# Performance work log

Hardware: AMD Instinct MI355X
Metric: run time of the kernel (lower is better)

## Reference

```python
import jax, jax.numpy as jnp
import numpy as np

N, D, K = 500000, 64, 256
INIT_COUNT = 100  # torch module initializes counts to 100 per cluster


def setup_inputs() -> dict:
    key = jax.random.key(0)
    k1, k2 = jax.random.split(key)
    embedded = jax.random.normal(k1, (N, D), dtype=jnp.float32)
    centers = jax.random.normal(k2, (K, D), dtype=jnp.float32)
    counts = jnp.ones((K,), dtype=jnp.int32) * INIT_COUNT
    return {"embedded": embedded, "centers": centers, "counts": counts}


def reference(embedded, centers, counts):
    # predict_hard: squared euclidean cdist + argmin over clusters
    x2 = jnp.sum(embedded * embedded, axis=1, keepdims=True)          # [N,1]
    c2 = jnp.sum(centers * centers, axis=1)                           # [K]
    dist = x2 - 2.0 * jnp.einsum('nd,kd->nk', embedded, centers) + c2  # [N,K]
    labels = jnp.argmin(dist, axis=1).astype(jnp.int32)               # [N]

    # dcn_loss: gather assigned center, squared diff, sum / N
    diff = embedded - centers[labels]                                 # [N,D]
    loss = jnp.sum(diff * diff) / embedded.shape[0]

    # update_centroids: the sequential running-mean update
    #   center = (1 - 1/count) * center + (1/count) * x  (count incremented per sample)
    # telescopes exactly to a segment-sum form:
    #   new_center_c = (counts_old[c]*center_c + sum_{i: label_i=c} x_i) / (counts_old[c] + n_c)
    n_clusters = centers.shape[0]
    seg_sum = jax.ops.segment_sum(embedded, labels, num_segments=n_clusters)  # [K,D]
    seg_cnt = jax.ops.segment_sum(jnp.ones_like(labels), labels, num_segments=n_clusters)  # [K] int32
    new_counts = counts + seg_cnt
    old_w = counts.astype(embedded.dtype)[:, None]
    new_w = new_counts.astype(embedded.dtype)[:, None]
    new_centers = (old_w * centers + seg_sum) / new_w
    return labels, loss, new_centers, new_counts
```

## Files before the change

kernel.cpp:

```cpp
#include <hip/hip_runtime.h>


typedef __attribute__((ext_vector_type(8))) short bf16x8;
typedef __attribute__((ext_vector_type(4))) float f32x4;

constexpr int K = 256;
constexpr int D = 64;
constexpr int BLK = 768;
constexpr int GRID = 256;
constexpr int WPB = BLK / 64;

struct alignas(16) PackW { unsigned int w[4]; };

#define DS_ADD_F32(addr32, val) \
  asm volatile("ds_add_f32 %0, %1" :: "v"(addr32), "v"(val))

__device__ __forceinline__ unsigned int pack_hi(unsigned int a, unsigned int b) {
  return (a >> 16) | (b & 0xffff0000u);
}

__device__ __forceinline__ void split8(const float4 a, const float4 b,
                                       bf16x8& s0, bf16x8& s1) {
  PackW p0, p1;
  const float fa[8] = {a.x, a.y, a.z, a.w, b.x, b.y, b.z, b.w};
#pragma unroll
  for (int i = 0; i < 4; ++i) {
    float f0 = fa[2 * i], f1 = fa[2 * i + 1];
    unsigned u0 = __float_as_uint(f0), u1 = __float_as_uint(f1);
    p0.w[i] = pack_hi(u0, u1);
    float r0 = f0 - __uint_as_float(u0 & 0xffff0000u);
    float r1 = f1 - __uint_as_float(u1 & 0xffff0000u);
    p1.w[i] = pack_hi(__float_as_uint(r0), __float_as_uint(r1));
  }
  s0 = __builtin_bit_cast(bf16x8, p0);
  s1 = __builtin_bit_cast(bf16x8, p1);
}

__global__ __launch_bounds__(BLK, 3) void assign_kernel(
    const float* __restrict__ emb,
    const float* __restrict__ centers,
    float* __restrict__ out_labels,
    float* __restrict__ ws_seg,
    int*   __restrict__ ws_cnt,
    float* __restrict__ ws_loss,
    int N)
{
  __shared__ __align__(16) unsigned short Bls[2 * K * D];
  __shared__ float seg_lds[K * D];
  __shared__ float hneg_lds[K];
  __shared__ int   cnt_lds[K];
  __shared__ float red[WPB];

  const int tid = threadIdx.x;

  for (int e = tid; e < K * D; e += BLK) {
    int j = e >> 6, d = e & 63;
    float cv = centers[e];
    unsigned u = __float_as_uint(cv);
    unsigned short h0 = (unsigned short)(u >> 16);
    float r = cv - __uint_as_float(u & 0xffff0000u);
    unsigned short h1 = (unsigned short)(__float_as_uint(r) >> 16);
    int nt = j >> 4, c = j & 15;
    int si = nt * 1024 + c * 64 + (d ^ ((c & 7) << 3));
    Bls[si] = h0;
    Bls[16384 + si] = h1;
  }
  if (tid < K) {
    const float4* cp = (const float4*)(centers + tid * D);
    float s = 0.f;
#pragma unroll
    for (int q = 0; q < 16; ++q) {
      float4 v = cp[q];
      s = fmaf(v.x, v.x, s); s = fmaf(v.y, v.y, s);
      s = fmaf(v.z, v.z, s); s = fmaf(v.w, v.w, s);
    }
    hneg_lds[tid] = -0.5f * s;
  }
  for (int e = tid; e < K * D; e += BLK) seg_lds[e] = 0.f;
  if (tid < K) cnt_lds[tid] = 0;
  __syncthreads();

  const int lane = tid & 63;
  const int wid  = tid >> 6;
  const int g    = lane >> 4;
  const int cc   = lane & 15;
  const int swzm = (cc & 7) << 3;
  const int bRow = cc * 64;
  const int bk0 = (8 * g) ^ swzm;
  const int bk1 = (32 + 8 * g) ^ swzm;

  float hreg[16];
#pragma unroll
  for (int nt = 0; nt < 16; ++nt) hreg[nt] = hneg_lds[nt * 16 + cc];

  const unsigned segbase = (unsigned)(size_t)seg_lds;

  float lossS = 0.f;
  float lossX = 0.f;
  const int TILES = N >> 5;
  const int waveGid = blockIdx.x * WPB + wid;

  for (int tile = waveGid; tile < TILES; tile += GRID * WPB) {
    const int base = tile << 5;

    float4 xa[2][2][2];
    bf16x8 fx[2][2][2];
#pragma unroll
    for (int Mt = 0; Mt < 2; ++Mt) {
#pragma unroll
      for (int ks = 0; ks < 2; ++ks) {
        const float4* rp = (const float4*)(emb + (size_t)(base + Mt * 16 + cc) * D + ks * 32 + g * 8);
        xa[Mt][ks][0] = rp[0];
        xa[Mt][ks][1] = rp[1];
      }
#pragma unroll
      for (int ks = 0; ks < 2; ++ks)
        split8(xa[Mt][ks][0], xa[Mt][ks][1], fx[Mt][ks][0], fx[Mt][ks][1]);
#pragma unroll
      for (int ks = 0; ks < 2; ++ks)
#pragma unroll
        for (int h = 0; h < 2; ++h) {
          float4 v = xa[Mt][ks][h];
          lossX = fmaf(v.x, v.x, lossX); lossX = fmaf(v.y, v.y, lossX);
          lossX = fmaf(v.z, v.z, lossX); lossX = fmaf(v.w, v.w, lossX);
        }
    }

    float bE[2][4];
#pragma unroll
    for (int Mt = 0; Mt < 2; ++Mt)
#pragma unroll
      for (int r = 0; r < 4; ++r) bE[Mt][r] = -3.0e38f;

    f32x4 accP[2];
#pragma unroll
    for (int nt = 0; nt < 16; ++nt) {
      float h = hreg[nt];
      f32x4 ci = {h, h, h, h};
      f32x4 a0, a1;
      {
        bf16x8 b0 = *(const bf16x8*)&Bls[nt * 1024 + bRow + bk0];
        bf16x8 b1 = *(const bf16x8*)&Bls[16384 + nt * 1024 + bRow + bk0];
        a0 = __builtin_amdgcn_mfma_f32_16x16x32_bf16(fx[0][0][0], b0, ci, 0, 0, 0);
        a0 = __builtin_amdgcn_mfma_f32_16x16x32_bf16(fx[0][0][1], b0, a0, 0, 0, 0);
        a0 = __builtin_amdgcn_mfma_f32_16x16x32_bf16(fx[0][0][0], b1, a0, 0, 0, 0);
        a1 = __builtin_amdgcn_mfma_f32_16x16x32_bf16(fx[1][0][0], b0, ci, 0, 0, 0);
        a1 = __builtin_amdgcn_mfma_f32_16x16x32_bf16(fx[1][0][1], b0, a1, 0, 0, 0);
        a1 = __builtin_amdgcn_mfma_f32_16x16x32_bf16(fx[1][0][0], b1, a1, 0, 0, 0);
      }
      {
        bf16x8 b0 = *(const bf16x8*)&Bls[nt * 1024 + bRow + bk1];
        bf16x8 b1 = *(const bf16x8*)&Bls[16384 + nt * 1024 + bRow + bk1];
        a0 = __builtin_amdgcn_mfma_f32_16x16x32_bf16(fx[0][1][0], b0, a0, 0, 0, 0);
        a0 = __builtin_amdgcn_mfma_f32_16x16x32_bf16(fx[0][1][1], b0, a0, 0, 0, 0);
        a0 = __builtin_amdgcn_mfma_f32_16x16x32_bf16(fx[0][1][0], b1, a0, 0, 0, 0);
        a1 = __builtin_amdgcn_mfma_f32_16x16x32_bf16(fx[1][1][0], b0, a1, 0, 0, 0);
        a1 = __builtin_amdgcn_mfma_f32_16x16x32_bf16(fx[1][1][1], b0, a1, 0, 0, 0);
        a1 = __builtin_amdgcn_mfma_f32_16x16x32_bf16(fx[1][1][0], b1, a1, 0, 0, 0);
      }
      if (nt > 0) {
        unsigned ib = (unsigned)cc | (unsigned)((nt - 1) << 4);
#pragma unroll
        for (int Mt = 0; Mt < 2; ++Mt)
#pragma unroll
          for (int r = 0; r < 4; ++r) {
            unsigned u = (__float_as_uint(accP[Mt][r]) & 0xFFFFFF00u) | ib;
            bE[Mt][r] = fmaxf(bE[Mt][r], __uint_as_float(u));
          }
      }
      accP[0] = a0; accP[1] = a1;
    }
    {
      unsigned ib = (unsigned)cc | (15u << 4);
#pragma unroll
      for (int Mt = 0; Mt < 2; ++Mt)
#pragma unroll
        for (int r = 0; r < 4; ++r) {
          unsigned u = (__float_as_uint(accP[Mt][r]) & 0xFFFFFF00u) | ib;
          bE[Mt][r] = fmaxf(bE[Mt][r], __uint_as_float(u));
        }
    }

#pragma unroll
    for (int Mt = 0; Mt < 2; ++Mt)
#pragma unroll
      for (int r = 0; r < 4; ++r)
#pragma unroll
        for (int m = 1; m <= 8; m <<= 1)
          bE[Mt][r] = fmaxf(bE[Mt][r], __shfl_xor(bE[Mt][r], m));

#pragma unroll
    for (int Mt = 0; Mt < 2; ++Mt) {
      float v01 = (cc & 1) ? bE[Mt][1] : bE[Mt][0];
      float v23 = (cc & 1) ? bE[Mt][3] : bE[Mt][2];
      float vv  = (cc & 2) ? v23 : v01;
      if (cc < 4) {
        int vi = (int)(__float_as_uint(vv) & 255u);
        out_labels[base + Mt * 16 + g * 4 + cc] = (float)vi;
        lossS += vv;
        atomicAdd(&cnt_lds[vi], 1);
      }
      int srcl = (cc >> 2) << 4;
      float e0 = __shfl(bE[Mt][0], srcl);
      float e1 = __shfl(bE[Mt][1], srcl);
      float e2 = __shfl(bE[Mt][2], srcl);
      float e3 = __shfl(bE[Mt][3], srcl);
      float t01 = (cc & 1) ? e1 : e0;
      float t23 = (cc & 1) ? e3 : e2;
      float er  = (cc & 2) ? t23 : t01;
      int lbl = (int)(__float_as_uint(er) & 255u);
      unsigned sb = segbase + ((unsigned)lbl << 8);
      int sw = lbl & 31;
#pragma unroll
      for (int ks = 0; ks < 2; ++ks)
#pragma unroll
        for (int hf = 0; hf < 2; ++hf) {
          float4 v = xa[Mt][ks][hf];
          int d0 = ks * 32 + 8 * g + hf * 4;
          DS_ADD_F32(sb + (unsigned)(((d0 + 0) ^ sw) << 2), v.x);
          DS_ADD_F32(sb + (unsigned)(((d0 + 1) ^ sw) << 2), v.y);
          DS_ADD_F32(sb + (unsigned)(((d0 + 2) ^ sw) << 2), v.z);
          DS_ADD_F32(sb + (unsigned)(((d0 + 3) ^ sw) << 2), v.w);
        }
    }
  }

  asm volatile("s_waitcnt lgkmcnt(0)" ::: "memory");

  float acc = fmaf(-2.f, lossS, lossX);
#pragma unroll
  for (int off = 32; off > 0; off >>= 1) acc += __shfl_down(acc, off);
  if (lane == 0) red[wid] = acc;
  __syncthreads();
  if (tid == 0) {
    float t = 0.f;
#pragma unroll
    for (int w = 0; w < WPB; ++w) t += red[w];
    unsafeAtomicAdd(ws_loss, t);
  }
  for (int e = tid; e < K * D; e += BLK) {
    int k = e >> 6, d = e & 63;
    unsafeAtomicAdd(&ws_seg[e], seg_lds[(k << 6) + (d ^ (k & 31))]);
  }
  if (tid < K) atomicAdd(&ws_cnt[tid], cnt_lds[tid]);
}

__global__ void finalize_kernel(
    const float* __restrict__ centers,
    const int* __restrict__ counts,
    const float* __restrict__ ws_seg,
    const int* __restrict__ ws_cnt,
    const float* __restrict__ ws_loss,
    float* __restrict__ out_loss,
    float* __restrict__ out_centers,
    float* __restrict__ out_counts,
    int N)
{
  int idx = blockIdx.x * blockDim.x + threadIdx.x;
  if (idx < K * D) {
    int k = idx >> 6;
    float oldw = (float)counts[k];
    float neww = (float)(counts[k] + ws_cnt[k]);
    out_centers[idx] = fmaf(oldw, centers[idx], ws_seg[idx]) / neww;
  }
  if (idx < K) out_counts[idx] = (float)(counts[idx] + ws_cnt[idx]);
  if (idx == 0) out_loss[0] = ws_loss[0] / (float)N;
}

extern "C" void kernel_launch(void* const* d_in, const int* in_sizes, int n_in,
                              void* d_out, int out_size, void* d_ws, size_t ws_size,
                              hipStream_t stream) {
  const float* emb     = (const float*)d_in[0];
  const float* centers = (const float*)d_in[1];
  const int*   counts  = (const int*)d_in[2];

  const int Kn = in_sizes[2];
  const int Dn = in_sizes[1] / Kn;
  const int N  = in_sizes[0] / Dn;

  float* out         = (float*)d_out;
  float* out_labels  = out;
  float* out_loss    = out + N;
  float* out_centers = out + N + 1;
  float* out_counts  = out + N + 1 + (size_t)Kn * Dn;

  float* ws_seg  = (float*)d_ws;
  int*   ws_cnt  = (int*)(ws_seg + (size_t)Kn * Dn);
  float* ws_loss = (float*)(ws_cnt + Kn);

  hipMemsetAsync(d_ws, 0, (size_t)(Kn * Dn + Kn + 1) * sizeof(float), stream);

  hipLaunchKernelGGL(assign_kernel, dim3(GRID), dim3(BLK), 0, stream,
                     emb, centers, out_labels, ws_seg, ws_cnt, ws_loss, N);

  hipLaunchKernelGGL(finalize_kernel, dim3((Kn * Dn + 255) / 256), dim3(256), 0, stream,
                     centers, counts, ws_seg, ws_cnt, ws_loss,
                     out_loss, out_centers, out_counts, N);
}
```

Baseline: 394.5 us.

## Split segment-sum out of assign kernel into separate pass for occupancy

Moves the per-cluster segment sum and count accumulation out of the distance/argmin kernel into a new segsum_kernel that re-reads embeddings and the just-written labels. Removing the 64KB seg_lds buffer from the assign kernel frees LDS, so the kernel can use 1024-thread blocks and a larger grid. The MFMA loop is also simplified by dropping the one-step delayed argmax pipelining. The cost is a second full pass over the 128MB embedding array plus an extra kernel launch.

```diff
diff --git a/kernel.cpp b/kernel.cpp
--- a/kernel.cpp
+++ b/kernel.cpp
@@ -6,9 +6,13 @@
 
 constexpr int K = 256;
 constexpr int D = 64;
-constexpr int BLK = 768;
-constexpr int GRID = 256;
-constexpr int WPB = BLK / 64;
+
+constexpr int BLK_A = 1024;
+constexpr int GRID_A = 512;
+constexpr int WPB_A = BLK_A / 64;
+
+constexpr int BLK_B = 1024;
+constexpr int GRID_B = 256;
 
 struct alignas(16) PackW { unsigned int w[4]; };
 
@@ -36,24 +40,20 @@
   s1 = __builtin_bit_cast(bf16x8, p1);
 }
 
-__global__ __launch_bounds__(BLK, 3) void assign_kernel(
+__global__ __launch_bounds__(BLK_A, 8) void assign_kernel(
     const float* __restrict__ emb,
     const float* __restrict__ centers,
     float* __restrict__ out_labels,
-    float* __restrict__ ws_seg,
-    int*   __restrict__ ws_cnt,
     float* __restrict__ ws_loss,
     int N)
 {
   __shared__ __align__(16) unsigned short Bls[2 * K * D];
-  __shared__ float seg_lds[K * D];
   __shared__ float hneg_lds[K];
-  __shared__ int   cnt_lds[K];
-  __shared__ float red[WPB];
+  __shared__ float red[WPB_A];
 
   const int tid = threadIdx.x;
 
-  for (int e = tid; e < K * D; e += BLK) {
+  for (int e = tid; e < K * D; e += BLK_A) {
     int j = e >> 6, d = e & 63;
     float cv = centers[e];
     unsigned u = __float_as_uint(cv);
@@ -76,8 +76,6 @@
     }
     hneg_lds[tid] = -0.5f * s;
   }
-  for (int e = tid; e < K * D; e += BLK) seg_lds[e] = 0.f;
-  if (tid < K) cnt_lds[tid] = 0;
   __syncthreads();
 
   const int lane = tid & 63;
@@ -93,14 +91,10 @@
 #pragma unroll
   for (int nt = 0; nt < 16; ++nt) hreg[nt] = hneg_lds[nt * 16 + cc];
 
-  const unsigned segbase = (unsigned)(size_t)seg_lds;
-
-  float lossS = 0.f;
-  float lossX = 0.f;
+  float lossS = 0.f, lossX = 0.f;
   const int TILES = N >> 5;
-  const int waveGid = blockIdx.x * WPB + wid;
-
-  for (int tile = waveGid; tile < TILES; tile += GRID * WPB) {
+
+  for (int tile = blockIdx.x * WPB_A + wid; tile < TILES; tile += GRID_A * WPB_A) {
     const int base = tile << 5;
 
     float4 xa[2][2][2];
@@ -132,53 +126,34 @@
 #pragma unroll
       for (int r = 0; r < 4; ++r) bE[Mt][r] = -3.0e38f;
 
-    f32x4 accP[2];
 #pragma unroll
     for (int nt = 0; nt < 16; ++nt) {
       float h = hreg[nt];
       f32x4 ci = {h, h, h, h};
+      bf16x8 b00 = *(const bf16x8*)&Bls[nt * 1024 + bRow + bk0];
+      bf16x8 b01 = *(const bf16x8*)&Bls[16384 + nt * 1024 + bRow + bk0];
+      bf16x8 b10 = *(const bf16x8*)&Bls[nt * 1024 + bRow + bk1];
+      bf16x8 b11 = *(const bf16x8*)&Bls[16384 + nt * 1024 + bRow + bk1];
       f32x4 a0, a1;
-      {
-        bf16x8 b0 = *(const bf16x8*)&Bls[nt * 1024 + bRow + bk0];
-        bf16x8 b1 = *(const bf16x8*)&Bls[16384 + nt * 1024 + bRow + bk0];
-        a0 = __builtin_amdgcn_mfma_f32_16x16x32_bf16(fx[0][0][0], b0, ci, 0, 0, 0);
-        a0 = __builtin_amdgcn_mfma_f32_16x16x32_bf16(fx[0][0][1], b0, a0, 0, 0, 0);
-        a0 = __builtin_amdgcn_mfma_f32_16x16x32_bf16(fx[0][0][0], b1, a0, 0, 0, 0);
-        a1 = __builtin_amdgcn_mfma_f32_16x16x32_bf16(fx[1][0][0], b0, ci, 0, 0, 0);
-        a1 = __builtin_amdgcn_mfma_f32_16x16x32_bf16(fx[1][0][1], b0, a1, 0, 0, 0);
-        a1 = __builtin_amdgcn_mfma_f32_16x16x32_bf16(fx[1][0][0], b1, a1, 0, 0, 0);
+      a0 = __builtin_amdgcn_mfma_f32_16x16x32_bf16(fx[0][0][0], b00, ci, 0, 0, 0);
+      a0 = __builtin_amdgcn_mfma_f32_16x16x32_bf16(fx[0][0][1], b00, a0, 0, 0, 0);
+      a0 = __builtin_amdgcn_mfma_f32_16x16x32_bf16(fx[0][0][0], b01, a0, 0, 0, 0);
+      a0 = __builtin_amdgcn_mfma_f32_16x16x32_bf16(fx[0][1][0], b10, a0, 0, 0, 0);
+      a0 = __builtin_amdgcn_mfma_f32_16x16x32_bf16(fx[0][1][1], b10, a0, 0, 0, 0);
+      a0 = __builtin_amdgcn_mfma_f32_16x16x32_bf16(fx[0][1][0], b11, a0, 0, 0, 0);
+      a1 = __builtin_amdgcn_mfma_f32_16x16x32_bf16(fx[1][0][0], b00, ci, 0, 0, 0);
+      a1 = __builtin_amdgcn_mfma_f32_16x16x32_bf16(fx[1][0][1], b00, a1, 0, 0, 0);
+      a1 = __builtin_amdgcn_mfma_f32_16x16x32_bf16(fx[1][0][0], b01, a1, 0, 0, 0);
+      a1 = __builtin_amdgcn_mfma_f32_16x16x32_bf16(fx[1][1][0], b10, a1, 0, 0, 0);
+      a1 = __builtin_amdgcn_mfma_f32_16x16x32_bf16(fx[1][1][1], b10, a1, 0, 0, 0);
+      a1 = __builtin_amdgcn_mfma_f32_16x16x32_bf16(fx[1][1][0], b11, a1, 0, 0, 0);
+
+      unsigned ib = (unsigned)(nt << 4) | (unsigned)cc;
+#pragma unroll
+      for (int r = 0; r < 4; ++r) {
+        bE[0][r] = fmaxf(bE[0][r], __uint_as_float((__float_as_uint(a0[r]) & 0xFFFFFF00u) | ib));
+        bE[1][r] = fmaxf(bE[1][r], __uint_as_float((__float_as_uint(a1[r]) & 0xFFFFFF00u) | ib));
       }
-      {
-        bf16x8 b0 = *(const bf16x8*)&Bls[nt * 1024 + bRow + bk1];
-        bf16x8 b1 = *(const bf16x8*)&Bls[16384 + nt * 1024 + bRow + bk1];
-        a0 = __builtin_amdgcn_mfma_f32_16x16x32_bf16(fx[0][1][0], b0, a0, 0, 0, 0);
-        a0 = __builtin_amdgcn_mfma_f32_16x16x32_bf16(fx[0][1][1], b0, a0, 0, 0, 0);
-        a0 = __builtin_amdgcn_mfma_f32_16x16x32_bf16(fx[0][1][0], b1, a0, 0, 0, 0);
-        a1 = __builtin_amdgcn_mfma_f32_16x16x32_bf16(fx[1][1][0], b0, a1, 0, 0, 0);
-        a1 = __builtin_amdgcn_mfma_f32_16x16x32_bf16(fx[1][1][1], b0, a1, 0, 0, 0);
-        a1 = __builtin_amdgcn_mfma_f32_16x16x32_bf16(fx[1][1][0], b1, a1, 0, 0, 0);
-      }
-      if (nt > 0) {
-        unsigned ib = (unsigned)cc | (unsigned)((nt - 1) << 4);
-#pragma unroll
-        for (int Mt = 0; Mt < 2; ++Mt)
-#pragma unroll
-          for (int r = 0; r < 4; ++r) {
-            unsigned u = (__float_as_uint(accP[Mt][r]) & 0xFFFFFF00u) | ib;
-            bE[Mt][r] = fmaxf(bE[Mt][r], __uint_as_float(u));
-          }
-      }
-      accP[0] = a0; accP[1] = a1;
-    }
-    {
-      unsigned ib = (unsigned)cc | (15u << 4);
-#pragma unroll
-      for (int Mt = 0; Mt < 2; ++Mt)
-#pragma unroll
-        for (int r = 0; r < 4; ++r) {
-          unsigned u = (__float_as_uint(accP[Mt][r]) & 0xFFFFFF00u) | ib;
-          bE[Mt][r] = fmaxf(bE[Mt][r], __uint_as_float(u));
-        }
     }
 
 #pragma unroll
@@ -198,34 +173,9 @@
         int vi = (int)(__float_as_uint(vv) & 255u);
         out_labels[base + Mt * 16 + g * 4 + cc] = (float)vi;
         lossS += vv;
-        atomicAdd(&cnt_lds[vi], 1);
       }
-      int srcl = (cc >> 2) << 4;
-      float e0 = __shfl(bE[Mt][0], srcl);
-      float e1 = __shfl(bE[Mt][1], srcl);
-      float e2 = __shfl(bE[Mt][2], srcl);
-      float e3 = __shfl(bE[Mt][3], srcl);
-      float t01 = (cc & 1) ? e1 : e0;
-      float t23 = (cc & 1) ? e3 : e2;
-      float er  = (cc & 2) ? t23 : t01;
-      int lbl = (int)(__float_as_uint(er) & 255u);
-      unsigned sb = segbase + ((unsigned)lbl << 8);
-      int sw = lbl & 31;
-#pragma unroll
-      for (int ks = 0; ks < 2; ++ks)
-#pragma unroll
-        for (int hf = 0; hf < 2; ++hf) {
-          float4 v = xa[Mt][ks][hf];
-          int d0 = ks * 32 + 8 * g + hf * 4;
-          DS_ADD_F32(sb + (unsigned)(((d0 + 0) ^ sw) << 2), v.x);
-          DS_ADD_F32(sb + (unsigned)(((d0 + 1) ^ sw) << 2), v.y);
-          DS_ADD_F32(sb + (unsigned)(((d0 + 2) ^ sw) << 2), v.z);
-          DS_ADD_F32(sb + (unsigned)(((d0 + 3) ^ sw) << 2), v.w);
-        }
     }
   }
-
-  asm volatile("s_waitcnt lgkmcnt(0)" ::: "memory");
 
   float acc = fmaf(-2.f, lossS, lossX);
 #pragma unroll
@@ -235,10 +185,60 @@
   if (tid == 0) {
     float t = 0.f;
 #pragma unroll
-    for (int w = 0; w < WPB; ++w) t += red[w];
+    for (int w = 0; w < WPB_A; ++w) t += red[w];
     unsafeAtomicAdd(ws_loss, t);
   }
-  for (int e = tid; e < K * D; e += BLK) {
+}
+
+__global__ __launch_bounds__(BLK_B, 8) void segsum_kernel(
+    const float* __restrict__ emb,
+    const float* __restrict__ labels_f,
+    float* __restrict__ ws_seg,
+    int*   __restrict__ ws_cnt,
+    int N)
+{
+  __shared__ float seg_lds[K * D];
+  __shared__ int   cnt_lds[K];
+
+  const int tid = threadIdx.x;
+  for (int e = tid; e < K * D; e += BLK_B) seg_lds[e] = 0.f;
+  if (tid < K) cnt_lds[tid] = 0;
+  __syncthreads();
+
+  const unsigned segbase = (unsigned)(size_t)seg_lds;
+  const int q = tid & 3;
+  const int SPP = GRID_B * BLK_B / 4;
+
+  for (int s = (blockIdx.x * BLK_B + tid) >> 2; s < N; s += SPP) {
+    int lbl = (int)labels_f[s];
+    const float4* rp = (const float4*)(emb + (size_t)s * D + q * 16);
+    float4 v0 = rp[0], v1 = rp[1], v2 = rp[2], v3 = rp[3];
+    unsigned sb = segbase + ((unsigned)lbl << 8);
+    int sw = lbl & 31;
+    int d0 = q * 16;
+    DS_ADD_F32(sb + (unsigned)(((d0 +  0) ^ sw) << 2), v0.x);
+    DS_ADD_F32(sb + (unsigned)(((d0 +  1) ^ sw) << 2), v0.y);
+    DS_ADD_F32(sb + (unsigned)(((d0 +  2) ^ sw) << 2), v0.z);
+    DS_ADD_F32(sb + (unsigned)(((d0 +  3) ^ sw) << 2), v0.w);
+    DS_ADD_F32(sb + (unsigned)(((d0 +  4) ^ sw) << 2), v1.x);
+    DS_ADD_F32(sb + (unsigned)(((d0 +  5) ^ sw) << 2), v1.y);
+    DS_ADD_F32(sb + (unsigned)(((d0 +  6) ^ sw) << 2), v1.z);
+    DS_ADD_F32(sb + (unsigned)(((d0 +  7) ^ sw) << 2), v1.w);
+    DS_ADD_F32(sb + (unsigned)(((d0 +  8) ^ sw) << 2), v2.x);
+    DS_ADD_F32(sb + (unsigned)(((d0 +  9) ^ sw) << 2), v2.y);
+    DS_ADD_F32(sb + (unsigned)(((d0 + 10) ^ sw) << 2), v2.z);
+    DS_ADD_F32(sb + (unsigned)(((d0 + 11) ^ sw) << 2), v2.w);
+    DS_ADD_F32(sb + (unsigned)(((d0 + 12) ^ sw) << 2), v3.x);
+    DS_ADD_F32(sb + (unsigned)(((d0 + 13) ^ sw) << 2), v3.y);
+    DS_ADD_F32(sb + (unsigned)(((d0 + 14) ^ sw) << 2), v3.z);
+    DS_ADD_F32(sb + (unsigned)(((d0 + 15) ^ sw) << 2), v3.w);
+    if (q == 0) atomicAdd(&cnt_lds[lbl], 1);
+  }
+
+  asm volatile("s_waitcnt lgkmcnt(0)" ::: "memory");
+  __syncthreads();
+
+  for (int e = tid; e < K * D; e += BLK_B) {
     int k = e >> 6, d = e & 63;
     unsafeAtomicAdd(&ws_seg[e], seg_lds[(k << 6) + (d ^ (k & 31))]);
   }
@@ -290,8 +290,11 @@
 
   hipMemsetAsync(d_ws, 0, (size_t)(Kn * Dn + Kn + 1) * sizeof(float), stream);
 
-  hipLaunchKernelGGL(assign_kernel, dim3(GRID), dim3(BLK), 0, stream,
-                     emb, centers, out_labels, ws_seg, ws_cnt, ws_loss, N);
+  hipLaunchKernelGGL(assign_kernel, dim3(GRID_A), dim3(BLK_A), 0, stream,
+                     emb, centers, out_labels, ws_loss, N);
+
+  hipLaunchKernelGGL(segsum_kernel, dim3(GRID_B), dim3(BLK_B), 0, stream,
+                     emb, out_labels, ws_seg, ws_cnt, N);
 
   hipLaunchKernelGGL(finalize_kernel, dim3((Kn * Dn + 255) / 256), dim3(256), 0, stream,
                      centers, counts, ws_seg, ws_cnt, ws_loss,
```

Measured after the change: 992.7 us. 152% more time.
